# Performance work log

Hardware: AMD Instinct MI355X
Metric: run time of the kernel (lower is better)

Reference implementation:

```python
import jax, jax.numpy as jnp
import numpy as np

SEQ, EMB, QKV = 4096, 1024, 1024

def setup_inputs() -> dict:
    key = jax.random.key(0)
    k_x, k_q, k_k, k_v = jax.random.split(key, 4)
    scale = 1.0 / np.sqrt(EMB)
    return {
        "x": jax.random.normal(k_x, (SEQ, EMB), dtype=jnp.float32),
        "W_q": jax.random.normal(k_q, (EMB, QKV), dtype=jnp.float32) * scale,
        "W_k": jax.random.normal(k_k, (EMB, QKV), dtype=jnp.float32) * scale,
        "W_v": jax.random.normal(k_v, (EMB, QKV), dtype=jnp.float32) * scale,
    }

def reference(x, W_q, W_k, W_v):
    # Single-head scaled dot-product attention, unbatched: x [S, E]
    d_k = W_q.shape[1]
    Q = x @ W_q          # [S, D]
    K = x @ W_k          # [S, D]
    V = x @ W_v          # [S, D]
    scores = (Q @ K.T) * (1.0 / jnp.sqrt(jnp.asarray(d_k, dtype=x.dtype)))  # [S, S]
    attn = jax.nn.softmax(scores, axis=-1)
    return attn @ V      # [S, D]
```

## Files before the change

kernel.cpp:

```cpp
#include <hip/hip_runtime.h>
#include <cstdint>

#define S_DIM 4096
#define E_DIM 1024
#define D_DIM 1024

typedef __bf16 bf16x8 __attribute__((ext_vector_type(8)));
typedef float  f32x4  __attribute__((ext_vector_type(4)));
typedef unsigned short u16x8 __attribute__((ext_vector_type(8)));

__device__ __forceinline__ unsigned short f2bf(float f) {
  unsigned u = __float_as_uint(f);
  unsigned r = (u + 0x7fffu + ((u >> 16) & 1u)) >> 16;
  return (unsigned short)r;
}

__device__ __forceinline__ void lds_copy16(const unsigned short* g, const unsigned short* l) {
  auto gp = reinterpret_cast<__attribute__((address_space(1))) unsigned int*>(
      reinterpret_cast<uintptr_t>(g));
  auto lp = reinterpret_cast<__attribute__((address_space(3))) unsigned int*>(
      reinterpret_cast<uintptr_t>(l));
  __builtin_amdgcn_global_load_lds(gp, lp, 16, 0, 0);
}

__global__ __launch_bounds__(256) void prep_kernel(
    const float* __restrict__ x,
    const float* __restrict__ Wq, const float* __restrict__ Wk, const float* __restrict__ Wv,
    unsigned short* __restrict__ xbf, unsigned short* __restrict__ Wt,
    float* __restrict__ lsum) {
  const int z = blockIdx.z;
  const int tid = threadIdx.x;
  if (z < 3) {
    const float* W = (z == 0) ? Wq : (z == 1 ? Wk : Wv);
    unsigned short* out = Wt + (size_t)z * E_DIM * D_DIM;
    __shared__ unsigned short tile[64][68];
    const int bc = blockIdx.x * 64;
    const int br = blockIdx.y * 64;
    const int tx = tid & 63, ty = tid >> 6;
#pragma unroll
    for (int i = 0; i < 64; i += 4)
      tile[tx][ty + i] = f2bf(W[(size_t)(br + ty + i) * D_DIM + bc + tx]);
    __syncthreads();
    const int dr = tid >> 4, eg = tid & 15;
#pragma unroll
    for (int i = 0; i < 64; i += 16)
      *(unsigned long long*)(out + (size_t)(bc + dr + i) * E_DIM + br + eg * 4) =
          *(const unsigned long long*)(&tile[dr + i][eg * 4]);
  } else {
    int bid = blockIdx.y * 16 + blockIdx.x;
#pragma unroll
    for (int s = 0; s < 4; ++s) {
      int i = ((bid * 4 + s) * 256 + tid) * 16;
#pragma unroll
      for (int h = 0; h < 2; h++) {
        float4 a = *(const float4*)(x + i + h * 8);
        float4 b = *(const float4*)(x + i + h * 8 + 4);
        u16x8 o;
        o[0] = f2bf(a.x); o[1] = f2bf(a.y); o[2] = f2bf(a.z); o[3] = f2bf(a.w);
        o[4] = f2bf(b.x); o[5] = f2bf(b.y); o[6] = f2bf(b.z); o[7] = f2bf(b.w);
        *(u16x8*)(xbf + i + h * 8) = o;
      }
    }
    if (bid < 16) lsum[bid * 256 + tid] = 0.f;
  }
}

template <int MODE, int NSPLIT, int BN, int BK>
__device__ __forceinline__ void gemm_body(
    const unsigned short* __restrict__ A, int lda,
    const unsigned short* __restrict__ Bt, int ldb,
    void* __restrict__ Cp, unsigned short* __restrict__ C1, int ldc,
    int Kper, float scale, float* __restrict__ lsum,
    int bm, int bn, unsigned short* sA, unsigned short* sB) {
  constexpr int NF = BN / 32;
  constexpr int NC = BK / 8;
  constexpr int RP = 2048 / BK;
  constexpr int PA = 128 / RP;
  constexpr int PB = BN / RP;
  constexpr int HH = BK / 32;

  const int tid = threadIdx.x;
  const int wave = tid >> 6;
  const int lane = tid & 63;
  const int q    = lane >> 4;
  const int l16  = lane & 15;
  const int lx   = l16 & (NC - 1);
  const int wm   = (wave >> 1) * 64;
  const int wn   = (wave & 1) * (BN / 2);

  f32x4 zero = {0.f, 0.f, 0.f, 0.f};
  f32x4 acc[4][NF];
#pragma unroll
  for (int t = 0; t < 4; t++)
#pragma unroll
    for (int u = 0; u < NF; u++) acc[t][u] = zero;

  const int srow   = tid / NC;
  const int schunk = (tid % NC) ^ (srow & (NC - 1));
  const unsigned short* ap = A  + (size_t)(bm + srow) * lda + schunk * 8;
  const unsigned short* bp = Bt + (size_t)(bn + srow) * ldb + schunk * 8;
  unsigned short* saw = sA + wave * 512;
  unsigned short* sbw = sB + wave * 512;
  const size_t stepA = (size_t)RP * lda;
  const size_t stepB = (size_t)RP * ldb;

  for (int k0 = 0; k0 < Kper; k0 += BK) {
#pragma unroll
    for (int p = 0; p < PA; p++)
      lds_copy16(ap + k0 + p * stepA, saw + p * 2048);
#pragma unroll
    for (int p = 0; p < PB; p++)
      lds_copy16(bp + k0 + p * stepB, sbw + p * 2048);
    __syncthreads();

#pragma unroll
    for (int h = 0; h < HH; h++) {
      bf16x8 af[4], bfv[NF];
      const int pc = (((h << 2) | q) ^ lx) * 8;
#pragma unroll
      for (int t = 0; t < 4; t++)
        af[t] = *reinterpret_cast<const bf16x8*>(sA + (wm + t * 16 + l16) * BK + pc);
#pragma unroll
      for (int u = 0; u < NF; u++)
        bfv[u] = *reinterpret_cast<const bf16x8*>(sB + (wn + u * 16 + l16) * BK + pc);
#pragma unroll
      for (int t = 0; t < 4; t++)
#pragma unroll
        for (int u = 0; u < NF; u++)
          acc[t][u] = __builtin_amdgcn_mfma_f32_16x16x32_bf16(af[t], bfv[u], acc[t][u], 0, 0, 0);
    }
    __syncthreads();
  }

  unsigned short* cb16 = (unsigned short*)Cp;
  int coloff = bn;
  if constexpr (NSPLIT == 2) {
    if (bn >= 1024) cb16 = C1;
    coloff = bn & 1023;
  }
  float* o32 = (float*)Cp;

#pragma unroll
  for (int t = 0; t < 4; t++) {
#pragma unroll
    for (int rr = 0; rr < 4; rr++) {
      const int row = bm + wm + t * 16 + q * 4 + rr;
      float invl = 1.0f;
      if constexpr (MODE == 2) invl = 1.0f / lsum[row];
      float rs = 0.f;
#pragma unroll
      for (int u = 0; u < NF; u++) {
        const int col = coloff + wn + u * 16 + l16;
        float v = acc[t][u][rr] * scale;
        if constexpr (MODE == 0) {
          cb16[(size_t)row * ldc + col] = f2bf(v);
        } else if constexpr (MODE == 1) {
          float p = __expf(v - 8.0f);
          rs += p;
          cb16[(size_t)row * ldc + col] = f2bf(p);
        } else {
          o32[(size_t)row * ldc + col] = acc[t][u][rr] * invl;
        }
      }
      if constexpr (MODE == 1) {
        rs += __shfl_xor(rs, 1);
        rs += __shfl_xor(rs, 2);
        rs += __shfl_xor(rs, 4);
        rs += __shfl_xor(rs, 8);
        if (l16 == 0) unsafeAtomicAdd(&lsum[row], rs);
      }
    }
  }
}

__global__ __launch_bounds__(256, 2) void qk_gemm(
    const unsigned short* __restrict__ xbf, const unsigned short* __restrict__ Wt,
    unsigned short* __restrict__ Qbf, unsigned short* __restrict__ Kbf) {
  __shared__ __align__(16) unsigned short sA[128 * 128];
  __shared__ __align__(16) unsigned short sB[128 * 128];
  const int bid = blockIdx.x;
  const int xcd = bid & 7, j = bid >> 3;
  const int bm = ((xcd & 3) * 8 + (j >> 3)) * 128;
  const int bn = ((xcd >> 2) * 8 + (j & 7)) * 128;
  gemm_body<0, 2, 128, 128>(xbf, E_DIM, Wt, E_DIM, Qbf, Kbf, D_DIM,
                            E_DIM, 1.0f, nullptr, bm, bn, sA, sB);
}

__global__ __launch_bounds__(256, 2) void sv_gemm(
    const unsigned short* __restrict__ xbf, const unsigned short* __restrict__ Wt,
    const unsigned short* __restrict__ Qbf, const unsigned short* __restrict__ Kbf,
    unsigned short* __restrict__ Vt, unsigned short* __restrict__ SP,
    float* __restrict__ lsum) {
  __shared__ __align__(16) unsigned short sA[128 * 64];
  __shared__ __align__(16) unsigned short sB[128 * 64];
  const int bid = blockIdx.x;
  if (bid < 256) {
    const int xcd = bid & 7, j = bid >> 3;
    const int bm = (j & 7) * 128;
    const int bn = (xcd * 4 + (j >> 3)) * 128;
    gemm_body<0, 1, 128, 64>(Wt + 2 * E_DIM * D_DIM, E_DIM, xbf, E_DIM, Vt,
                             nullptr, S_DIM, E_DIM, 1.0f, nullptr, bm, bn, sA, sB);
  } else {
    const int idx = bid - 256;
    const int xcd = idx & 7, j = idx >> 3;
    const int bm = ((xcd & 1) * 16 + (j >> 3)) * 128;
    const int bn = ((xcd >> 1) * 8 + (j & 7)) * 128;
    gemm_body<1, 1, 128, 64>(Qbf, D_DIM, Kbf, D_DIM, SP, nullptr, S_DIM,
                             D_DIM, 0.03125f, lsum, bm, bn, sA, sB);
  }
}

__global__ __launch_bounds__(256, 2) void o_gemm(
    const unsigned short* __restrict__ SP, const unsigned short* __restrict__ Vt,
    float* __restrict__ out, const float* __restrict__ lsum) {
  __shared__ __align__(16) unsigned short sA[128 * 128];
  __shared__ __align__(16) unsigned short sB[64 * 128];
  int flat = blockIdx.y * gridDim.x + blockIdx.x;
  int numInG = 8 * gridDim.x;
  int g = flat / numInG;
  int r = flat - g * numInG;
  int bm = (g * 8 + (r & 7)) * 128, bn = (r >> 3) * 64;
  gemm_body<2, 1, 64, 128>(SP, S_DIM, Vt, S_DIM, out, nullptr, D_DIM,
                           S_DIM, 1.0f, (float*)lsum, bm, bn, sA, sB);
}

extern "C" void kernel_launch(void* const* d_in, const int* in_sizes, int n_in,
                              void* d_out, int out_size, void* d_ws, size_t ws_size,
                              hipStream_t stream) {
  const float* x  = (const float*)d_in[0];
  const float* Wq = (const float*)d_in[1];
  const float* Wk = (const float*)d_in[2];
  const float* Wv = (const float*)d_in[3];
  float* out = (float*)d_out;

  char* ws = (char*)d_ws;
  const size_t MB = 1024 * 1024;
  unsigned short* SP   = (unsigned short*)(ws);
  unsigned short* xbf  = (unsigned short*)(ws + 8 * MB);
  unsigned short* Wt   = (unsigned short*)(ws + 16 * MB);
  unsigned short* Qbf  = (unsigned short*)(ws + 32 * MB);
  unsigned short* Kbf  = (unsigned short*)(ws + 40 * MB);
  unsigned short* Vt   = (unsigned short*)(ws + 48 * MB);
  float*          lsum = (float*)(ws + 56 * MB);

  dim3 blk(256);

  dim3 prgrid(16, 16, 4);
  prep_kernel<<<prgrid, blk, 0, stream>>>(x, Wq, Wk, Wv, xbf, Wt, lsum);

  qk_gemm<<<dim3(512), blk, 0, stream>>>(xbf, Wt, Qbf, Kbf);

  sv_gemm<<<dim3(1280), blk, 0, stream>>>(xbf, Wt, Qbf, Kbf, Vt, SP, lsum);

  dim3 ogrid(16, 32);
  o_gemm<<<ogrid, blk, 0, stream>>>(SP, Vt, out, lsum);
}
```

Measured before the change: 200.2 us.

## Split-K the PV GEMM into two halves with a separate normalize-reduce kernel

```diff
diff --git a/kernel.cpp b/kernel.cpp
--- a/kernel.cpp
+++ b/kernel.cpp
@@ -31,6 +31,7 @@
   const int z = blockIdx.z;
   const int tid = threadIdx.x;
   if (z < 3) {
+    if (blockIdx.x >= 16) return;
     const float* W = (z == 0) ? Wq : (z == 1 ? Wk : Wv);
     unsigned short* out = Wt + (size_t)z * E_DIM * D_DIM;
     __shared__ unsigned short tile[64][68];
@@ -47,10 +48,10 @@
       *(unsigned long long*)(out + (size_t)(bc + dr + i) * E_DIM + br + eg * 4) =
           *(const unsigned long long*)(&tile[dr + i][eg * 4]);
   } else {
-    int bid = blockIdx.y * 16 + blockIdx.x;
-#pragma unroll
-    for (int s = 0; s < 4; ++s) {
-      int i = ((bid * 4 + s) * 256 + tid) * 16;
+    int bid = blockIdx.y * 32 + blockIdx.x;
+#pragma unroll
+    for (int s = 0; s < 2; ++s) {
+      int i = ((bid * 2 + s) * 256 + tid) * 16;
 #pragma unroll
       for (int h = 0; h < 2; h++) {
         float4 a = *(const float4*)(x + i + h * 8);
@@ -145,8 +146,6 @@
 #pragma unroll
     for (int rr = 0; rr < 4; rr++) {
       const int row = bm + wm + t * 16 + q * 4 + rr;
-      float invl = 1.0f;
-      if constexpr (MODE == 2) invl = 1.0f / lsum[row];
       float rs = 0.f;
 #pragma unroll
       for (int u = 0; u < NF; u++) {
@@ -159,7 +158,7 @@
           rs += p;
           cb16[(size_t)row * ldc + col] = f2bf(p);
         } else {
-          o32[(size_t)row * ldc + col] = acc[t][u][rr] * invl;
+          o32[(size_t)row * ldc + col] = v;
         }
       }
       if constexpr (MODE == 1) {
@@ -212,16 +211,36 @@
 
 __global__ __launch_bounds__(256, 2) void o_gemm(
     const unsigned short* __restrict__ SP, const unsigned short* __restrict__ Vt,
-    float* __restrict__ out, const float* __restrict__ lsum) {
+    float* __restrict__ Prt, float* __restrict__ out) {
   __shared__ __align__(16) unsigned short sA[128 * 128];
   __shared__ __align__(16) unsigned short sB[64 * 128];
-  int flat = blockIdx.y * gridDim.x + blockIdx.x;
-  int numInG = 8 * gridDim.x;
-  int g = flat / numInG;
-  int r = flat - g * numInG;
-  int bm = (g * 8 + (r & 7)) * 128, bn = (r >> 3) * 64;
-  gemm_body<2, 1, 64, 128>(SP, S_DIM, Vt, S_DIM, out, nullptr, D_DIM,
-                           S_DIM, 1.0f, (float*)lsum, bm, bn, sA, sB);
+  const int bid = blockIdx.x;
+  const int kh = bid & 1;
+  const int flat = bid >> 1;
+  const int g = flat >> 7, r = flat & 127;
+  const int bm = (g * 8 + (r & 7)) * 128, bn = (r >> 3) * 64;
+  float* dst = kh ? out : Prt;
+  gemm_body<2, 1, 64, 128>(SP + kh * 2048, S_DIM, Vt + kh * 2048, S_DIM,
+                           dst, nullptr, D_DIM, 2048, 1.0f, nullptr,
+                           bm, bn, sA, sB);
+}
+
+__global__ __launch_bounds__(256) void reduce_out_kernel(
+    float* __restrict__ out, const float* __restrict__ part,
+    const float* __restrict__ lsum) {
+  const int n4 = (S_DIM * D_DIM) >> 2;
+  const int stride = gridDim.x * blockDim.x;
+  for (int v = blockIdx.x * blockDim.x + threadIdx.x; v < n4; v += stride) {
+    float inv = 1.0f / lsum[v >> 8];
+    float4 a = reinterpret_cast<const float4*>(out)[v];
+    float4 b = reinterpret_cast<const float4*>(part)[v];
+    float4 o;
+    o.x = (a.x + b.x) * inv;
+    o.y = (a.y + b.y) * inv;
+    o.z = (a.z + b.z) * inv;
+    o.w = (a.w + b.w) * inv;
+    reinterpret_cast<float4*>(out)[v] = o;
+  }
 }
 
 extern "C" void kernel_launch(void* const* d_in, const int* in_sizes, int n_in,
@@ -241,17 +260,19 @@
   unsigned short* Qbf  = (unsigned short*)(ws + 32 * MB);
   unsigned short* Kbf  = (unsigned short*)(ws + 40 * MB);
   unsigned short* Vt   = (unsigned short*)(ws + 48 * MB);
+  float*          Prt  = (float*)(ws + 32 * MB);
   float*          lsum = (float*)(ws + 56 * MB);
 
   dim3 blk(256);
 
-  dim3 prgrid(16, 16, 4);
+  dim3 prgrid(32, 16, 4);
   prep_kernel<<<prgrid, blk, 0, stream>>>(x, Wq, Wk, Wv, xbf, Wt, lsum);
 
   qk_gemm<<<dim3(512), blk, 0, stream>>>(xbf, Wt, Qbf, Kbf);
 
   sv_gemm<<<dim3(1280), blk, 0, stream>>>(xbf, Wt, Qbf, Kbf, Vt, SP, lsum);
 
-  dim3 ogrid(16, 32);
-  o_gemm<<<ogrid, blk, 0, stream>>>(SP, Vt, out, lsum);
-}
+  o_gemm<<<dim3(1024), blk, 0, stream>>>(SP, Vt, Prt, out);
+
+  reduce_out_kernel<<<dim3(2048), blk, 0, stream>>>(out, Prt, lsum);
+}
```

New measurement: 206.6 us. 3.2% more time.
